# Kernel optimization log

Hardware: AMD Instinct MI355X
Metric: run time of the kernel (lower is better)

The kernel has to match this reference:

```python
import jax, jax.numpy as jnp
import numpy as np

B, V, NB, NJ, NEXTRA = 512, 6890, 10, 24, 9
PARENTS = np.array([-1,0,0,0,1,2,3,4,5,6,7,8,9,9,9,12,13,14,16,17,18,19,20,21], dtype=np.int32)


def setup_inputs() -> dict:
    key = jax.random.key(0)
    ks = jax.random.split(key, 11)
    betas = jax.random.normal(ks[0], (B, NB + 1), jnp.float32) * 0.1
    betas = betas.at[:, 0].set(1.0)  # col 0 is a global scale in this SMPL variant
    body_pose = jax.random.normal(ks[1], (B, 3 * (NJ - 1)), jnp.float32) * 0.2
    global_orient = jax.random.normal(ks[2], (B, 3), jnp.float32) * 0.2
    transl = jax.random.normal(ks[3], (B, 3), jnp.float32) * 0.1
    model_scale_opt = jnp.ones((1,), jnp.float32)
    smpl_v_template = jax.random.normal(ks[4], (V, 3), jnp.float32)
    smil_v_template = jax.random.normal(ks[5], (V, 3), jnp.float32)
    shapedirs = jax.random.normal(ks[6], (V, 3, NB), jnp.float32) * 0.01
    J_regressor = jax.nn.softmax(jax.random.normal(ks[7], (NJ, V), jnp.float32), axis=1)
    lbs_weights = jax.nn.softmax(jax.random.normal(ks[8], (V, NJ), jnp.float32) * 4.0, axis=1)
    J_regressor_extra = jax.nn.softmax(jax.random.normal(ks[9], (NEXTRA, V), jnp.float32), axis=1)
    parents = jnp.asarray(PARENTS)
    return dict(betas=betas, body_pose=body_pose, global_orient=global_orient,
                transl=transl, model_scale_opt=model_scale_opt,
                smpl_v_template=smpl_v_template, smil_v_template=smil_v_template,
                shapedirs=shapedirs, J_regressor=J_regressor, lbs_weights=lbs_weights,
                J_regressor_extra=J_regressor_extra, parents=parents)


def batch_rodrigues(rvecs):
    # rvecs: [N,3] axis-angle -> [N,3,3] rotation matrices
    angle = jnp.linalg.norm(rvecs + 1e-8, axis=1, keepdims=True)  # [N,1]
    axis = rvecs / angle
    c = jnp.cos(angle)[..., None]  # [N,1,1]
    s = jnp.sin(angle)[..., None]
    rx, ry, rz = axis[:, 0], axis[:, 1], axis[:, 2]
    z = jnp.zeros_like(rx)
    K = jnp.stack([z, -rz, ry, rz, z, -rx, -ry, rx, z], axis=1).reshape(-1, 3, 3)
    I = jnp.eye(3, dtype=rvecs.dtype)
    return I + s * K + (1.0 - c) * jnp.matmul(K, K)


def _smpl_forward(betas, body_pose, global_orient, transl, model_scale_opt,
                  smpl_v_template, smil_v_template, shapedirs,
                  J_regressor, lbs_weights, J_regressor_extra):
    dtype = betas.dtype
    # ---- updateShape ----
    s = model_scale_opt[0]
    v_template = smpl_v_template * s + (1.0 - s) * smil_v_template  # [V,3]
    blend_shape = jnp.einsum('bl,mkl->bmk', betas[:, 1:], shapedirs)  # [B,V,3]
    v_shaped = (v_template[None] + blend_shape) * betas[:, :1, None]  # scale col
    J_shaped = jnp.einsum('bik,ji->bjk', v_shaped, J_regressor)  # [B,NJ,3]

    # ---- updatePose ----
    full_pose = jnp.concatenate([global_orient, body_pose], axis=1)  # [B,NJ*3]
    rot_mats = batch_rodrigues(full_pose.reshape(-1, 3)).reshape(B, NJ, 3, 3)

    # relative joint locations w.r.t. parents
    rel_joints = J_shaped.at[:, 1:].add(-J_shaped[:, PARENTS[1:]])
    top = jnp.concatenate([rot_mats, rel_joints[..., None]], axis=-1)  # [B,NJ,3,4]
    bottom = jnp.broadcast_to(
        jnp.array([0.0, 0.0, 0.0, 1.0], dtype=dtype), (B, NJ, 1, 4))
    mats = jnp.concatenate([top, bottom], axis=2)  # [B,NJ,4,4]

    # sequential kinematic-chain composition over the 24-joint tree
    chain = [mats[:, 0]]
    for i in range(1, NJ):
        chain.append(jnp.matmul(chain[PARENTS[i]], mats[:, i]))
    chain = jnp.stack(chain, axis=1)  # [B,NJ,4,4]
    posed_joints = chain[:, :, :3, 3]  # [B,NJ,3]

    # relative transforms: subtract rotated rest joints
    corr = jnp.einsum('bjmn,bjn->bjm', chain[:, :, :3, :3], J_shaped)
    A = chain.at[:, :, :3, 3].add(-corr)  # [B,NJ,4,4]

    # linear blend skinning
    T = jnp.einsum('vj,bjmn->bvmn', lbs_weights, A)  # [B,V,4,4]
    verts = jnp.einsum('bvmn,bvn->bvm', T[:, :, :3, :3], v_shaped) + T[:, :, :3, 3]

    extra_joints = jnp.einsum('bik,ji->bjk', verts, J_regressor_extra)  # [B,9,3]
    joints = jnp.concatenate([posed_joints, extra_joints], axis=1)  # [B,33,3]

    t = transl[:, None, :]
    # concat verts and joints along point dim for a single output array
    return jnp.concatenate([verts + t, joints + t], axis=1)  # [B, V+33, 3]


def reference(betas, body_pose, global_orient, transl, model_scale_opt,
              smpl_v_template, smil_v_template, shapedirs,
              J_regressor, lbs_weights, J_regressor_extra, parents):
    return _smpl_forward(betas, body_pose, global_orient, transl, model_scale_opt,
                         smpl_v_template, smil_v_template, shapedirs,
                         J_regressor, lbs_weights, J_regressor_extra)
```

## Files before the change

### kernel.cpp

```cpp
#include <hip/hip_runtime.h>


#define BATCH 512
#define NV 6890
#define NBD 10
#define NJ 24
#define NEXTRA 9
#define NOUT (NV + NJ + NEXTRA)
#define VBLK ((NV + 255) / 256)
#define BPB 4
#define PCHUNK 8
#define PCLEN ((NV + PCHUNK - 1) / PCHUNK)
#define EPN 34

__constant__ int c_par[NJ] = {-1,0,0,0,1,2,3,4,5,6,7,8,9,9,9,12,13,14,16,17,18,19,20,21};
__constant__ int c_dep[NJ] = {0,1,1,1,2,2,2,3,3,3,4,4,4,4,4,5,5,5,6,6,7,7,8,8};

__global__ __launch_bounds__(256) void pre_kernel(
    const float* __restrict__ jreg,
    const float* __restrict__ jre,
    const float* __restrict__ lbsw,
    const float* __restrict__ smpl_t,
    const float* __restrict__ smil_t,
    const float* __restrict__ sdirs,
    const float* __restrict__ msc,
    float* __restrict__ jtjs_part,
    float* __restrict__ epre)
{
    const int j = blockIdx.y;
    const float s = msc[0];

    __shared__ float red[4][EPN];
    const int lane = threadIdx.x & 63, wv = threadIdx.x >> 6;

    if (blockIdx.x < PCHUNK) {
        const int c = blockIdx.x;
        const int vbeg = c * PCLEN;
        const int vend_ = (vbeg + PCLEN < NV) ? vbeg + PCLEN : NV;

        float acc[33];
#pragma unroll
        for (int i = 0; i < 33; ++i) acc[i] = 0.f;

        for (int v = vbeg + threadIdx.x; v < vend_; v += 256) {
            const float w = jreg[j * NV + v];
#pragma unroll
            for (int k = 0; k < 3; ++k) {
                float vt = s * smpl_t[v * 3 + k] + (1.f - s) * smil_t[v * 3 + k];
                acc[k] = fmaf(w, vt, acc[k]);
            }
            const float2* sd2 = (const float2*)(sdirs + (size_t)v * 30);
#pragma unroll
            for (int i = 0; i < 15; ++i) {
                float2 x = sd2[i];
                acc[3 + 2 * i]     = fmaf(w, x.x, acc[3 + 2 * i]);
                acc[3 + 2 * i + 1] = fmaf(w, x.y, acc[3 + 2 * i + 1]);
            }
        }

#pragma unroll
        for (int i = 0; i < 33; ++i) {
            float x = acc[i];
            for (int off = 32; off; off >>= 1) x += __shfl_xor(x, off, 64);
            acc[i] = x;
        }
        if (lane == 0) {
#pragma unroll
            for (int i = 0; i < 33; ++i) red[wv][i] = acc[i];
        }
        __syncthreads();
        if (threadIdx.x < 33) {
            jtjs_part[(c * NJ + j) * 33 + threadIdx.x] =
                red[0][threadIdx.x] + red[1][threadIdx.x]
              + red[2][threadIdx.x] + red[3][threadIdx.x];
        }
    } else {
        const int e = blockIdx.x - PCHUNK;

        float acc[EPN];
#pragma unroll
        for (int i = 0; i < EPN; ++i) acc[i] = 0.f;

        for (int v = threadIdx.x; v < NV; v += 256) {
            const float u = jre[e * NV + v] * lbsw[(size_t)v * NJ + j];
            acc[33] += u;
#pragma unroll
            for (int k = 0; k < 3; ++k) {
                float vt = s * smpl_t[v * 3 + k] + (1.f - s) * smil_t[v * 3 + k];
                acc[k] = fmaf(u, vt, acc[k]);
            }
            const float2* sd2 = (const float2*)(sdirs + (size_t)v * 30);
#pragma unroll
            for (int i = 0; i < 15; ++i) {
                float2 x = sd2[i];
                acc[3 + 2 * i]     = fmaf(u, x.x, acc[3 + 2 * i]);
                acc[3 + 2 * i + 1] = fmaf(u, x.y, acc[3 + 2 * i + 1]);
            }
        }

#pragma unroll
        for (int i = 0; i < EPN; ++i) {
            float x = acc[i];
            for (int off = 32; off; off >>= 1) x += __shfl_xor(x, off, 64);
            acc[i] = x;
        }
        if (lane == 0) {
#pragma unroll
            for (int i = 0; i < EPN; ++i) red[wv][i] = acc[i];
        }
        __syncthreads();
        if (threadIdx.x < EPN) {
            epre[(e * NJ + j) * EPN + threadIdx.x] =
                red[0][threadIdx.x] + red[1][threadIdx.x]
              + red[2][threadIdx.x] + red[3][threadIdx.x];
        }
    }
}

__global__ __launch_bounds__(64) void joints_kernel(
    const float* __restrict__ betas,
    const float* __restrict__ body_pose,
    const float* __restrict__ glob_or,
    const float* __restrict__ transl,
    const float* __restrict__ jtjs_part,
    const float* __restrict__ epre,
    float* __restrict__ wsA,
    float* __restrict__ out)
{
    const int b = blockIdx.x;
    const int j = threadIdx.x;

    __shared__ float sJ[NJ][3];
    __shared__ float mats[NJ][12];
    __shared__ float chain[NJ][12];
    __shared__ float sbeta[NBD + 1];
    __shared__ float sS[NEXTRA][NJ][3];
    __shared__ float sW[NEXTRA][NJ];

    if (threadIdx.x < NBD + 1) sbeta[threadIdx.x] = betas[b * (NBD + 1) + threadIdx.x];
    __syncthreads();

    if (j < NJ) {
        float jt[33];
#pragma unroll
        for (int i = 0; i < 33; ++i) jt[i] = 0.f;
        for (int c = 0; c < PCHUNK; ++c) {
#pragma unroll
            for (int i = 0; i < 33; ++i) jt[i] += jtjs_part[(c * NJ + j) * 33 + i];
        }

        const float beta0 = sbeta[0];
#pragma unroll
        for (int k = 0; k < 3; ++k) {
            float a = jt[k];
#pragma unroll
            for (int l = 0; l < NBD; ++l) a = fmaf(sbeta[1 + l], jt[3 + k * 10 + l], a);
            sJ[j][k] = a * beta0;
        }
        float rx, ry, rz;
        if (j == 0) {
            rx = glob_or[b * 3 + 0]; ry = glob_or[b * 3 + 1]; rz = glob_or[b * 3 + 2];
        } else {
            rx = body_pose[b * 69 + (j - 1) * 3 + 0];
            ry = body_pose[b * 69 + (j - 1) * 3 + 1];
            rz = body_pose[b * 69 + (j - 1) * 3 + 2];
        }
        float ex = rx + 1e-8f, ey = ry + 1e-8f, ez = rz + 1e-8f;
        float ang = sqrtf(ex * ex + ey * ey + ez * ez);
        float inv = 1.f / ang;
        float ax = rx * inv, ay = ry * inv, az = rz * inv;
        float c = cosf(ang), s = sinf(ang), t = 1.f - c;
        mats[j][0]  = 1.f + t * (-(ay * ay + az * az));
        mats[j][1]  = -s * az + t * (ax * ay);
        mats[j][2]  =  s * ay + t * (ax * az);
        mats[j][4]  =  s * az + t * (ax * ay);
        mats[j][5]  = 1.f + t * (-(ax * ax + az * az));
        mats[j][6]  = -s * ax + t * (ay * az);
        mats[j][8]  = -s * ay + t * (ax * az);
        mats[j][9]  =  s * ax + t * (ay * az);
        mats[j][10] = 1.f + t * (-(ax * ax + ay * ay));
    }
    __syncthreads();
    if (j < NJ) {
        const int p = c_par[j];
        float t0 = sJ[j][0], t1 = sJ[j][1], t2 = sJ[j][2];
        if (p >= 0) { t0 -= sJ[p][0]; t1 -= sJ[p][1]; t2 -= sJ[p][2]; }
        mats[j][3] = t0; mats[j][7] = t1; mats[j][11] = t2;
    }
    __syncthreads();
    if (j == 0) {
#pragma unroll
        for (int k = 0; k < 12; ++k) chain[0][k] = mats[0][k];
    }
    __syncthreads();
    for (int lev = 1; lev <= 8; ++lev) {
        if (j < NJ && c_dep[j] == lev) {
            const int p = c_par[j];
            float r_[12];
#pragma unroll
            for (int r = 0; r < 3; ++r) {
#pragma unroll
                for (int col = 0; col < 4; ++col) {
                    float acc = (col == 3) ? chain[p][r * 4 + 3] : 0.f;
#pragma unroll
                    for (int q = 0; q < 3; ++q) acc = fmaf(chain[p][r * 4 + q], mats[j][q * 4 + col], acc);
                    r_[r * 4 + col] = acc;
                }
            }
#pragma unroll
            for (int k = 0; k < 12; ++k) chain[j][k] = r_[k];
        }
        __syncthreads();
    }
    if (j < NJ) {
        float A[12];
#pragma unroll
        for (int k = 0; k < 12; ++k) A[k] = chain[j][k];
        const float c0 = A[3], c1 = A[7], c2 = A[11];
        const float j0 = sJ[j][0], j1 = sJ[j][1], j2 = sJ[j][2];
        A[3]  = c0 - (A[0] * j0 + A[1] * j1 + A[2]  * j2);
        A[7]  = c1 - (A[4] * j0 + A[5] * j1 + A[6]  * j2);
        A[11] = c2 - (A[8] * j0 + A[9] * j1 + A[10] * j2);
#pragma unroll
        for (int k = 0; k < 12; ++k) wsA[((size_t)b * NJ + j) * 12 + k] = A[k];
#pragma unroll
        for (int k = 0; k < 12; ++k) mats[j][k] = A[k];
        const float tx = transl[b * 3 + 0], ty = transl[b * 3 + 1], tz = transl[b * 3 + 2];
        const size_t o = ((size_t)b * NOUT + NV + j) * 3;
        out[o + 0] = c0 + tx; out[o + 1] = c1 + ty; out[o + 2] = c2 + tz;
    }

    for (int idx = threadIdx.x; idx < NEXTRA * NJ * 3; idx += 64) {
        const int e  = idx / (NJ * 3);
        const int r  = idx - e * NJ * 3;
        const int jj = r / 3;
        const int cc = r - jj * 3;
        const float* ep = epre + (e * NJ + jj) * EPN;
        float a = ep[cc];
#pragma unroll
        for (int l = 0; l < NBD; ++l) a = fmaf(sbeta[1 + l], ep[3 + cc * 10 + l], a);
        sS[e][jj][cc] = a * sbeta[0];
    }
    for (int idx = threadIdx.x; idx < NEXTRA * NJ; idx += 64) {
        const int e  = idx / NJ;
        const int jj = idx - e * NJ;
        sW[e][jj] = epre[(e * NJ + jj) * EPN + 33];
    }
    __syncthreads();
    if (threadIdx.x < 3 * NEXTRA) {
        const int e = threadIdx.x / 3;
        const int k = threadIdx.x - e * 3;
        float acc = 0.f;
#pragma unroll 4
        for (int jj = 0; jj < NJ; ++jj) {
            acc = fmaf(mats[jj][k * 4 + 0], sS[e][jj][0], acc);
            acc = fmaf(mats[jj][k * 4 + 1], sS[e][jj][1], acc);
            acc = fmaf(mats[jj][k * 4 + 2], sS[e][jj][2], acc);
            acc = fmaf(mats[jj][k * 4 + 3], sW[e][jj],    acc);
        }
        out[((size_t)b * NOUT + NV + NJ) * 3 + threadIdx.x] = acc + transl[b * 3 + k];
    }
}

__global__ __launch_bounds__(256) void lbs_kernel(
    const float* __restrict__ betas,
    const float* __restrict__ transl,
    const float* __restrict__ msc,
    const float* __restrict__ smpl_t,
    const float* __restrict__ smil_t,
    const float* __restrict__ sdirs,
    const float* __restrict__ lbsw,
    const float* __restrict__ wsA,
    float* __restrict__ out)
{
    const int v = blockIdx.x * 256 + threadIdx.x;
    const bool valid = v < NV;
    const int vc = valid ? v : NV - 1;
    const int b0 = blockIdx.y * BPB;
    const float s = msc[0];

    float vt[3];
#pragma unroll
    for (int k = 0; k < 3; ++k)
        vt[k] = s * smpl_t[vc * 3 + k] + (1.f - s) * smil_t[vc * 3 + k];

    float sd[30];
    {
        const float2* sd2 = (const float2*)(sdirs + (size_t)vc * 30);
#pragma unroll
        for (int i = 0; i < 15; ++i) { float2 x = sd2[i]; sd[2 * i] = x.x; sd[2 * i + 1] = x.y; }
    }
    float w[NJ];
    {
        const float4* w4 = (const float4*)(lbsw + (size_t)vc * NJ);
#pragma unroll
        for (int i = 0; i < 6; ++i) {
            float4 x = w4[i];
            w[4 * i] = x.x; w[4 * i + 1] = x.y; w[4 * i + 2] = x.z; w[4 * i + 3] = x.w;
        }
    }

#pragma unroll
    for (int bb = 0; bb < BPB; ++bb) {
        const int b = b0 + bb;
        const float* __restrict__ Bb = betas + b * (NBD + 1);
        const float* __restrict__ Ab = wsA + (size_t)b * NJ * 12;

        float vs[3];
#pragma unroll
        for (int k = 0; k < 3; ++k) {
            float a = vt[k];
#pragma unroll
            for (int l = 0; l < NBD; ++l) a = fmaf(Bb[1 + l], sd[k * 10 + l], a);
            vs[k] = a * Bb[0];
        }

        float T[12];
#pragma unroll
        for (int k = 0; k < 12; ++k) T[k] = 0.f;
#pragma unroll 4
        for (int jj = 0; jj < NJ; ++jj) {
            const float ww = w[jj];
#pragma unroll
            for (int k = 0; k < 12; ++k) T[k] = fmaf(ww, Ab[jj * 12 + k], T[k]);
        }

        if (valid) {
            const float tx = transl[b * 3 + 0], ty = transl[b * 3 + 1], tz = transl[b * 3 + 2];
            const size_t o = ((size_t)b * NOUT + v) * 3;
            out[o + 0] = fmaf(T[0], vs[0], fmaf(T[1], vs[1], fmaf(T[2],  vs[2], T[3])))  + tx;
            out[o + 1] = fmaf(T[4], vs[0], fmaf(T[5], vs[1], fmaf(T[6],  vs[2], T[7])))  + ty;
            out[o + 2] = fmaf(T[8], vs[0], fmaf(T[9], vs[1], fmaf(T[10], vs[2], T[11]))) + tz;
        }
    }
}

extern "C" void kernel_launch(void* const* d_in, const int* in_sizes, int n_in,
                              void* d_out, int out_size, void* d_ws, size_t ws_size,
                              hipStream_t stream) {
    const float* betas     = (const float*)d_in[0];
    const float* body_pose = (const float*)d_in[1];
    const float* glob_or   = (const float*)d_in[2];
    const float* transl    = (const float*)d_in[3];
    const float* msc       = (const float*)d_in[4];
    const float* smpl_t    = (const float*)d_in[5];
    const float* smil_t    = (const float*)d_in[6];
    const float* sdirs     = (const float*)d_in[7];
    const float* jreg      = (const float*)d_in[8];
    const float* lbsw      = (const float*)d_in[9];
    const float* jre       = (const float*)d_in[10];

    float* out  = (float*)d_out;
    float* ws   = (float*)d_ws;
    float* wsA       = ws;
    float* jtjs_part = wsA + (size_t)BATCH * NJ * 12;
    float* epre      = jtjs_part + PCHUNK * NJ * 33;

    dim3 gA(PCHUNK + NEXTRA, NJ);
    pre_kernel<<<gA, 256, 0, stream>>>(jreg, jre, lbsw, smpl_t, smil_t, sdirs, msc,
                                       jtjs_part, epre);

    joints_kernel<<<BATCH, 64, 0, stream>>>(betas, body_pose, glob_or, transl,
                                            jtjs_part, epre, wsA, out);

    dim3 gC(VBLK, BATCH / BPB);
    lbs_kernel<<<gC, 256, 0, stream>>>(betas, transl, msc, smpl_t, smil_t, sdirs, lbsw, wsA, out);
}
```

Before: 193.9 us.

## Stage skinning weights through shared memory and give each lbs block one batch

In the extra-joint precompute branch, each block now cooperatively loads 256-vertex tiles of the skinning weights into shared memory with float4 copies, replacing strided scalar global reads. The joints kernel merges its two epre loops into one per (e,j) pair. The LBS kernel drops its four-batches-per-block loop and processes one batch per block, quadrupling the grid. That gives more parallelism but reloads the per-vertex template, shapedirs and weights four times as often.

```diff
diff --git a/kernel.cpp b/kernel.cpp
--- a/kernel.cpp
+++ b/kernel.cpp
@@ -8,7 +8,6 @@
 #define NEXTRA 9
 #define NOUT (NV + NJ + NEXTRA)
 #define VBLK ((NV + 255) / 256)
-#define BPB 4
 #define PCHUNK 8
 #define PCLEN ((NV + PCHUNK - 1) / PCHUNK)
 #define EPN 34
@@ -30,6 +29,8 @@
     const int j = blockIdx.y;
     const float s = msc[0];
 
+    __shared__ float4 slw4[256 * NJ / 4];
+    float* slw = (float*)slw4;
     __shared__ float red[4][EPN];
     const int lane = threadIdx.x & 63, wv = threadIdx.x >> 6;
 
@@ -81,20 +82,30 @@
 #pragma unroll
         for (int i = 0; i < EPN; ++i) acc[i] = 0.f;
 
-        for (int v = threadIdx.x; v < NV; v += 256) {
-            const float u = jre[e * NV + v] * lbsw[(size_t)v * NJ + j];
-            acc[33] += u;
-#pragma unroll
-            for (int k = 0; k < 3; ++k) {
-                float vt = s * smpl_t[v * 3 + k] + (1.f - s) * smil_t[v * 3 + k];
-                acc[k] = fmaf(u, vt, acc[k]);
-            }
-            const float2* sd2 = (const float2*)(sdirs + (size_t)v * 30);
-#pragma unroll
-            for (int i = 0; i < 15; ++i) {
-                float2 x = sd2[i];
-                acc[3 + 2 * i]     = fmaf(u, x.x, acc[3 + 2 * i]);
-                acc[3 + 2 * i + 1] = fmaf(u, x.y, acc[3 + 2 * i + 1]);
+        for (int v0 = 0; v0 < NV; v0 += 256) {
+            const int nv = (NV - v0 < 256) ? (NV - v0) : 256;
+            __syncthreads();
+            {
+                const float4* src = (const float4*)(lbsw + (size_t)v0 * NJ);
+                for (int t = threadIdx.x; t < nv * 6; t += 256) slw4[t] = src[t];
+            }
+            __syncthreads();
+            const int v = v0 + (int)threadIdx.x;
+            if (v < NV) {
+                const float u = jre[e * NV + v] * slw[threadIdx.x * NJ + j];
+                acc[33] += u;
+#pragma unroll
+                for (int k = 0; k < 3; ++k) {
+                    float vt = s * smpl_t[v * 3 + k] + (1.f - s) * smil_t[v * 3 + k];
+                    acc[k] = fmaf(u, vt, acc[k]);
+                }
+                const float2* sd2 = (const float2*)(sdirs + (size_t)v * 30);
+#pragma unroll
+                for (int i = 0; i < 15; ++i) {
+                    float2 x = sd2[i];
+                    acc[3 + 2 * i]     = fmaf(u, x.x, acc[3 + 2 * i]);
+                    acc[3 + 2 * i + 1] = fmaf(u, x.y, acc[3 + 2 * i + 1]);
+                }
             }
         }
 
@@ -104,6 +115,7 @@
             for (int off = 32; off; off >>= 1) x += __shfl_xor(x, off, 64);
             acc[i] = x;
         }
+        __syncthreads();
         if (lane == 0) {
 #pragma unroll
             for (int i = 0; i < EPN; ++i) red[wv][i] = acc[i];
@@ -230,21 +242,18 @@
         out[o + 0] = c0 + tx; out[o + 1] = c1 + ty; out[o + 2] = c2 + tz;
     }
 
-    for (int idx = threadIdx.x; idx < NEXTRA * NJ * 3; idx += 64) {
-        const int e  = idx / (NJ * 3);
-        const int r  = idx - e * NJ * 3;
-        const int jj = r / 3;
-        const int cc = r - jj * 3;
-        const float* ep = epre + (e * NJ + jj) * EPN;
-        float a = ep[cc];
-#pragma unroll
-        for (int l = 0; l < NBD; ++l) a = fmaf(sbeta[1 + l], ep[3 + cc * 10 + l], a);
-        sS[e][jj][cc] = a * sbeta[0];
-    }
-    for (int idx = threadIdx.x; idx < NEXTRA * NJ; idx += 64) {
-        const int e  = idx / NJ;
-        const int jj = idx - e * NJ;
-        sW[e][jj] = epre[(e * NJ + jj) * EPN + 33];
+    for (int p = threadIdx.x; p < NEXTRA * NJ; p += 64) {
+        const int e  = p / NJ;
+        const int jj = p - e * NJ;
+        const float* ep = epre + p * EPN;
+#pragma unroll
+        for (int cc = 0; cc < 3; ++cc) {
+            float a = ep[cc];
+#pragma unroll
+            for (int l = 0; l < NBD; ++l) a = fmaf(sbeta[1 + l], ep[3 + cc * 10 + l], a);
+            sS[e][jj][cc] = a * sbeta[0];
+        }
+        sW[e][jj] = ep[33];
     }
     __syncthreads();
     if (threadIdx.x < 3 * NEXTRA) {
@@ -276,7 +285,7 @@
     const int v = blockIdx.x * 256 + threadIdx.x;
     const bool valid = v < NV;
     const int vc = valid ? v : NV - 1;
-    const int b0 = blockIdx.y * BPB;
+    const int b = blockIdx.y;
     const float s = msc[0];
 
     float vt[3];
@@ -300,38 +309,34 @@
         }
     }
 
-#pragma unroll
-    for (int bb = 0; bb < BPB; ++bb) {
-        const int b = b0 + bb;
-        const float* __restrict__ Bb = betas + b * (NBD + 1);
-        const float* __restrict__ Ab = wsA + (size_t)b * NJ * 12;
-
-        float vs[3];
-#pragma unroll
-        for (int k = 0; k < 3; ++k) {
-            float a = vt[k];
-#pragma unroll
-            for (int l = 0; l < NBD; ++l) a = fmaf(Bb[1 + l], sd[k * 10 + l], a);
-            vs[k] = a * Bb[0];
-        }
-
-        float T[12];
-#pragma unroll
-        for (int k = 0; k < 12; ++k) T[k] = 0.f;
+    const float* __restrict__ Bb = betas + b * (NBD + 1);
+    const float* __restrict__ Ab = wsA + (size_t)b * NJ * 12;
+
+    float vs[3];
+#pragma unroll
+    for (int k = 0; k < 3; ++k) {
+        float a = vt[k];
+#pragma unroll
+        for (int l = 0; l < NBD; ++l) a = fmaf(Bb[1 + l], sd[k * 10 + l], a);
+        vs[k] = a * Bb[0];
+    }
+
+    float T[12];
+#pragma unroll
+    for (int k = 0; k < 12; ++k) T[k] = 0.f;
 #pragma unroll 4
-        for (int jj = 0; jj < NJ; ++jj) {
-            const float ww = w[jj];
-#pragma unroll
-            for (int k = 0; k < 12; ++k) T[k] = fmaf(ww, Ab[jj * 12 + k], T[k]);
-        }
-
-        if (valid) {
-            const float tx = transl[b * 3 + 0], ty = transl[b * 3 + 1], tz = transl[b * 3 + 2];
-            const size_t o = ((size_t)b * NOUT + v) * 3;
-            out[o + 0] = fmaf(T[0], vs[0], fmaf(T[1], vs[1], fmaf(T[2],  vs[2], T[3])))  + tx;
-            out[o + 1] = fmaf(T[4], vs[0], fmaf(T[5], vs[1], fmaf(T[6],  vs[2], T[7])))  + ty;
-            out[o + 2] = fmaf(T[8], vs[0], fmaf(T[9], vs[1], fmaf(T[10], vs[2], T[11]))) + tz;
-        }
+    for (int jj = 0; jj < NJ; ++jj) {
+        const float ww = w[jj];
+#pragma unroll
+        for (int k = 0; k < 12; ++k) T[k] = fmaf(ww, Ab[jj * 12 + k], T[k]);
+    }
+
+    if (valid) {
+        const float tx = transl[b * 3 + 0], ty = transl[b * 3 + 1], tz = transl[b * 3 + 2];
+        const size_t o = ((size_t)b * NOUT + v) * 3;
+        out[o + 0] = fmaf(T[0], vs[0], fmaf(T[1], vs[1], fmaf(T[2],  vs[2], T[3])))  + tx;
+        out[o + 1] = fmaf(T[4], vs[0], fmaf(T[5], vs[1], fmaf(T[6],  vs[2], T[7])))  + ty;
+        out[o + 2] = fmaf(T[8], vs[0], fmaf(T[9], vs[1], fmaf(T[10], vs[2], T[11]))) + tz;
     }
 }
 
@@ -363,6 +368,6 @@
     joints_kernel<<<BATCH, 64, 0, stream>>>(betas, body_pose, glob_or, transl,
                                             jtjs_part, epre, wsA, out);
 
-    dim3 gC(VBLK, BATCH / BPB);
+    dim3 gC(VBLK, BATCH);
     lbs_kernel<<<gC, 256, 0, stream>>>(betas, transl, msc, smpl_t, smil_t, sdirs, lbsw, wsA, out);
 }
```

New measurement: 212.6 us. 1.1x slower.
